# Optimization experiments

Hardware: AMD Instinct MI355X
Metric: run time of the kernel (lower is better)

The kernel has to match this reference:

```python
import jax, jax.numpy as jnp
import numpy as np

ROI_SIZE = 14  # hard-coded in the torch module


def _bilinear(feature, x, y):
    """feature: [B,C,H,W]; x, y: arbitrary (matching) shape S of sample coords.
    Returns [B, C, *S]. Matches torch code: corner indices are clamped BEFORE
    the interpolation weights are computed from them."""
    H, W = feature.shape[-2:]
    y1 = jnp.clip(jnp.floor(y).astype(jnp.int32), 0, H - 1)
    y2 = jnp.clip(jnp.floor(y).astype(jnp.int32) + 1, 0, H - 1)
    x1 = jnp.clip(jnp.floor(x).astype(jnp.int32), 0, W - 1)
    x2 = jnp.clip(jnp.floor(x).astype(jnp.int32) + 1, 0, W - 1)
    wx_lo = x - x1  # weight toward x2 column
    wx_hi = x2 - x  # weight toward x1 column
    wy_lo = y - y1
    wy_hi = y2 - y
    p = feature[:, :, y1, x1] * wx_hi + feature[:, :, y1, x2] * wx_lo
    q = feature[:, :, y2, x1] * wx_hi + feature[:, :, y2, x2] * wx_lo
    return p * wy_hi + q * wy_lo


def setup_inputs() -> dict:
    key = jax.random.key(0)
    kf, k1, k2, k3, k4 = jax.random.split(key, 5)
    B, C, H, W, R = 1, 256, 200, 320, 128
    feature = jax.random.normal(kf, (B, C, H, W), dtype=jnp.float32)
    y1 = jax.random.uniform(k1, (R,), minval=0.0, maxval=H * 0.5)
    x1 = jax.random.uniform(k2, (R,), minval=0.0, maxval=W * 0.5)
    hh = jax.random.uniform(k3, (R,), minval=8.0, maxval=H * 0.45)
    ww = jax.random.uniform(k4, (R,), minval=8.0, maxval=W * 0.45)
    rois = jnp.stack([y1, x1, y1 + hh, x1 + ww], axis=-1).astype(jnp.float32)
    return {"feature": feature, "rois": rois}


def reference(feature, rois):
    R = rois.shape[0]
    B, C, H, W = feature.shape
    sh = (rois[:, 2] - rois[:, 0]) / ROI_SIZE  # [R] bin height stride
    sw = (rois[:, 3] - rois[:, 1]) / ROI_SIZE  # [R] bin width stride
    m = jnp.arange(ROI_SIZE, dtype=rois.dtype)
    y_base = rois[:, 0:1] + sh[:, None] * m  # [R, M]
    x_base = rois[:, 1:2] + sw[:, None] * m  # [R, N]
    frac = jnp.array([1.0 / 3.0, 2.0 / 3.0], dtype=rois.dtype)
    ys = y_base[:, :, None] + sh[:, None, None] * frac  # [R, M, 2]
    xs = x_base[:, :, None] + sw[:, None, None] * frac  # [R, N, 2]
    # all 4 (y, x) sample-point combos per bin -> [R, M, N, 2, 2]
    yy = jnp.broadcast_to(ys[:, :, None, :, None], (R, ROI_SIZE, ROI_SIZE, 2, 2))
    xx = jnp.broadcast_to(xs[:, None, :, None, :], (R, ROI_SIZE, ROI_SIZE, 2, 2))
    samples = _bilinear(feature, xx, yy)  # [B, C, R, M, N, 2, 2]
    # Faithful to torch.max(tensor) with NO dim: global max over B, C, R and
    # the 4 sample points, giving one scalar per bin (m, n).
    bin_max = jnp.max(samples, axis=(0, 1, 2, 5, 6))  # [M, N]
    return jnp.broadcast_to(bin_max, (R, C, ROI_SIZE, ROI_SIZE))
```

## Files before the change

kernel.cpp:

```cpp
#include <hip/hip_runtime.h>
#include <float.h>

#define CC 256
#define HH 200
#define WW 320
#define HW (HH * WW)
#define MM 14
#define CG 8
#define CPB (CC / CG)
#define CPW (CPB / 4)

__global__ void roi_init(float* __restrict__ binmax) {
    int t = blockIdx.x * blockDim.x + threadIdx.x;
    if (t < MM * MM) binmax[t] = -FLT_MAX;
}

__device__ inline void atomicMaxF(float* addr, float val) {
    if (val >= 0.0f) {
        atomicMax((int*)addr, __float_as_int(val));
    } else {
        atomicMin((unsigned int*)addr, __float_as_uint(val));
    }
}

__global__ __launch_bounds__(256) void roi_reduce(
    const float* __restrict__ feature,
    const float* __restrict__ rois,
    float* __restrict__ binmax)
{
    __shared__ float pmax[4][MM];

    const int bid = blockIdx.x;
    const int cg  = bid & (CG - 1);
    const int rm  = bid >> 3;
    const int m   = rm % MM;
    const int r   = rm / MM;
    const int tid  = threadIdx.x;
    const int w    = tid >> 6;
    const int lane = tid & 63;

    const float ry1 = rois[r * 4 + 0];
    const float rx1 = rois[r * 4 + 1];
    const float ry2 = rois[r * 4 + 2];
    const float rx2 = rois[r * 4 + 3];
    const float sh = (ry2 - ry1) * (1.0f / 14.0f);
    const float sw = (rx2 - rx1) * (1.0f / 14.0f);
    const float f13 = 1.0f / 3.0f, f23 = 2.0f / 3.0f;

    const int s = lane & 31;
    const int i = lane >> 5;
    const int n = s >> 1;
    const int j = s & 1;
    const bool active = s < 28;

    const float x = rx1 + sw * (float)n + sw * (j ? f23 : f13);
    const float y = ry1 + sh * (float)m + sh * (i ? f23 : f13);
    const int x1c = min(max((int)floorf(x), 0), WW - 1);
    const int x2c = min(max((int)floorf(x) + 1, 0), WW - 1);
    const int y1c = min(max((int)floorf(y), 0), HH - 1);
    const int y2c = min(max((int)floorf(y) + 1, 0), HH - 1);
    const float wxlo = x - (float)x1c, wxhi = (float)x2c - x;
    const float wylo = y - (float)y1c, wyhi = (float)y2c - y;

    int o11 = y1c * WW + x1c;
    int o12 = y1c * WW + x2c;
    int o21 = y2c * WW + x1c;
    int o22 = y2c * WW + x2c;
    if (!active) { o11 = o12 = o21 = o22 = 0; }

    const float* fbase = feature + (cg * CPB + w * CPW) * HW;

    float v11[CPW], v12[CPW], v21[CPW], v22[CPW];
    #pragma unroll
    for (int c = 0; c < CPW; ++c) {
        const float* fc = fbase + c * HW;
        v11[c] = fc[o11];
        v12[c] = fc[o12];
        v21[c] = fc[o21];
        v22[c] = fc[o22];
    }

    float lmax = -FLT_MAX;
    #pragma unroll
    for (int c = 0; c < CPW; ++c) {
        float p = v11[c] * wxhi + v12[c] * wxlo;
        float q = v21[c] * wxhi + v22[c] * wxlo;
        lmax = fmaxf(lmax, p * wyhi + q * wylo);
    }

    float v = lmax;
    v = fmaxf(v, __shfl_xor(v, 1));
    v = fmaxf(v, __shfl_xor(v, 32));
    if (active && j == 0 && i == 0) pmax[w][n] = v;
    __syncthreads();
    if (tid < MM) {
        float vv = fmaxf(fmaxf(pmax[0][tid], pmax[1][tid]),
                         fmaxf(pmax[2][tid], pmax[3][tid]));
        atomicMaxF(&binmax[m * MM + tid], vv);
    }
}

#define BCAST_BLOCKS 784
__global__ __launch_bounds__(256) void roi_bcast(
    const float* __restrict__ binmax, float4* __restrict__ out, int total4)
{
    const int idx0 = blockIdx.x * 256 + threadIdx.x;
    const float4 val = ((const float4*)binmax)[idx0 % 49];
    const int stride = BCAST_BLOCKS * 256;
    #pragma unroll
    for (int k = 0; k < 8; ++k) {
        int idx = idx0 + k * stride;
        if (idx < total4) out[idx] = val;
    }
}

extern "C" void kernel_launch(void* const* d_in, const int* in_sizes, int n_in,
                              void* d_out, int out_size, void* d_ws, size_t ws_size,
                              hipStream_t stream) {
    const float* feature = (const float*)d_in[0];
    const float* rois    = (const float*)d_in[1];
    float* binmax = (float*)d_ws;
    float* out    = (float*)d_out;

    const int R = in_sizes[1] / 4;

    roi_init<<<1, 256, 0, stream>>>(binmax);
    roi_reduce<<<R * MM * CG, 256, 0, stream>>>(feature, rois, binmax);

    const int total4 = out_size / 4;
    roi_bcast<<<BCAST_BLOCKS, 256, 0, stream>>>(binmax, (float4*)out, total4);
}
```

Measured before the change: 152.5 us.

## Transpose feature to channels-last in workspace for coalesced bilinear gathers

Adds a tiled shared-memory transpose that rewrites the NCHW feature map into an HWC copy in the workspace. A new reduce kernel then gathers the bilinear corners as contiguous float4 channel vectors and processes all 14 rows of an ROI per block, replacing the channel-strided scalar gathers. The cost is an extra full read and write of the feature map on every call. The new path needs a workspace of roughly 65 MB and falls back to the old kernel when the workspace is smaller.

```diff
diff --git a/kernel.cpp b/kernel.cpp
--- a/kernel.cpp
+++ b/kernel.cpp
@@ -10,6 +10,9 @@
 #define CPB (CC / CG)
 #define CPW (CPB / 4)
 
+#define WS_FT_OFF 1024
+#define FT_BYTES ((size_t)HW * CC * 4)
+
 __global__ void roi_init(float* __restrict__ binmax) {
     int t = blockIdx.x * blockDim.x + threadIdx.x;
     if (t < MM * MM) binmax[t] = -FLT_MAX;
@@ -23,13 +26,132 @@
     }
 }
 
-__global__ __launch_bounds__(256) void roi_reduce(
+__global__ __launch_bounds__(256) void roi_transpose(
+    const float* __restrict__ f, float* __restrict__ ft)
+{
+    __shared__ float tile[64][65];
+    const int gb = blockIdx.x;
+    const int h  = gb / 20;
+    const int rest = gb % 20;
+    const int wb = (rest / 4) * 64;
+    const int cb = (rest % 4) * 64;
+    const int tx = threadIdx.x & 63;
+    const int g  = threadIdx.x >> 6;
+    #pragma unroll
+    for (int k = 0; k < 16; ++k) {
+        int cl = g * 16 + k;
+        tile[cl][tx] = f[(cb + cl) * HW + h * WW + wb + tx];
+    }
+    __syncthreads();
+    #pragma unroll
+    for (int k = 0; k < 16; ++k) {
+        int wl = g * 16 + k;
+        ft[(h * WW + wb + wl) * CC + cb + tx] = tile[tx][wl];
+    }
+}
+
+__global__ __launch_bounds__(256) void roi_reduce_t(
+    const float* __restrict__ ft,
+    const float* __restrict__ rois,
+    float* __restrict__ binmax)
+{
+    __shared__ float pm[MM][MM][2];
+
+    const int bid = blockIdx.x;
+    const int cg  = bid & (CG - 1);
+    const int r   = bid >> 3;
+    const int tid  = threadIdx.x;
+    const int w    = tid >> 6;
+    const int lane = tid & 63;
+    const int iw    = w & 1;
+    const int nbase = (w >> 1) * 7;
+    const int s8 = lane >> 3;
+    const int c8 = lane & 7;
+    const int cgo = cg * 8 + c8;
+
+    const float ry1 = rois[r * 4 + 0];
+    const float rx1 = rois[r * 4 + 1];
+    const float ry2 = rois[r * 4 + 2];
+    const float rx2 = rois[r * 4 + 3];
+    const float sh = (ry2 - ry1) * (1.0f / 14.0f);
+    const float sw = (rx2 - rx1) * (1.0f / 14.0f);
+    const float f13 = 1.0f / 3.0f, f23 = 2.0f / 3.0f;
+    const float yfrac = iw ? f23 : f13;
+
+    const float4* f4 = (const float4*)ft;
+
+    float wxlo[2], wxhi[2];
+    int ox1[2], ox2[2];
+    bool val[2];
+    #pragma unroll
+    for (int p = 0; p < 2; ++p) {
+        const int ls = p * 8 + s8;
+        val[p] = ls < 14;
+        const int n = nbase + (ls >> 1);
+        const int j = ls & 1;
+        const float x = rx1 + sw * (float)n + sw * (j ? f23 : f13);
+        const int x1c = min(max((int)floorf(x), 0), WW - 1);
+        const int x2c = min(max((int)floorf(x) + 1, 0), WW - 1);
+        wxlo[p] = x - (float)x1c;
+        wxhi[p] = (float)x2c - x;
+        ox1[p] = val[p] ? x1c : 0;
+        ox2[p] = val[p] ? x2c : 0;
+    }
+
+    for (int m = 0; m < MM; ++m) {
+        const float y = ry1 + sh * (float)m + sh * yfrac;
+        const int y1c = min(max((int)floorf(y), 0), HH - 1);
+        const int y2c = min(max((int)floorf(y) + 1, 0), HH - 1);
+        const float wylo = y - (float)y1c, wyhi = (float)y2c - y;
+        const int row1 = y1c * WW, row2 = y2c * WW;
+
+        float4 v11[2], v12[2], v21[2], v22[2];
+        #pragma unroll
+        for (int p = 0; p < 2; ++p) {
+            v11[p] = f4[(row1 + ox1[p]) * 64 + cgo];
+            v12[p] = f4[(row1 + ox2[p]) * 64 + cgo];
+            v21[p] = f4[(row2 + ox1[p]) * 64 + cgo];
+            v22[p] = f4[(row2 + ox2[p]) * 64 + cgo];
+        }
+        #pragma unroll
+        for (int p = 0; p < 2; ++p) {
+            float px = v11[p].x * wxhi[p] + v12[p].x * wxlo[p];
+            float py = v11[p].y * wxhi[p] + v12[p].y * wxlo[p];
+            float pz = v11[p].z * wxhi[p] + v12[p].z * wxlo[p];
+            float pw = v11[p].w * wxhi[p] + v12[p].w * wxlo[p];
+            float qx = v21[p].x * wxhi[p] + v22[p].x * wxlo[p];
+            float qy = v21[p].y * wxhi[p] + v22[p].y * wxlo[p];
+            float qz = v21[p].z * wxhi[p] + v22[p].z * wxlo[p];
+            float qw = v21[p].w * wxhi[p] + v22[p].w * wxlo[p];
+            float rx = px * wyhi + qx * wylo;
+            float ry = py * wyhi + qy * wylo;
+            float rz = pz * wyhi + qz * wylo;
+            float rw = pw * wyhi + qw * wylo;
+            float sm = fmaxf(fmaxf(rx, ry), fmaxf(rz, rw));
+            if (!val[p]) sm = -FLT_MAX;
+            sm = fmaxf(sm, __shfl_xor(sm, 1));
+            sm = fmaxf(sm, __shfl_xor(sm, 2));
+            sm = fmaxf(sm, __shfl_xor(sm, 4));
+            sm = fmaxf(sm, __shfl_xor(sm, 8));
+            const int ls = p * 8 + s8;
+            if ((lane & 15) == 0 && val[p])
+                pm[m][nbase + (ls >> 1)][iw] = sm;
+        }
+    }
+
+    __syncthreads();
+    if (tid < MM * MM) {
+        float vv = fmaxf(pm[tid / MM][tid % MM][0], pm[tid / MM][tid % MM][1]);
+        atomicMaxF(&binmax[tid], vv);
+    }
+}
+
+__global__ __launch_bounds__(256) void roi_reduce_g(
     const float* __restrict__ feature,
     const float* __restrict__ rois,
     float* __restrict__ binmax)
 {
     __shared__ float pmax[4][MM];
-
     const int bid = blockIdx.x;
     const int cg  = bid & (CG - 1);
     const int rm  = bid >> 3;
@@ -62,24 +184,17 @@
     const float wxlo = x - (float)x1c, wxhi = (float)x2c - x;
     const float wylo = y - (float)y1c, wyhi = (float)y2c - y;
 
-    int o11 = y1c * WW + x1c;
-    int o12 = y1c * WW + x2c;
-    int o21 = y2c * WW + x1c;
-    int o22 = y2c * WW + x2c;
+    int o11 = y1c * WW + x1c, o12 = y1c * WW + x2c;
+    int o21 = y2c * WW + x1c, o22 = y2c * WW + x2c;
     if (!active) { o11 = o12 = o21 = o22 = 0; }
 
     const float* fbase = feature + (cg * CPB + w * CPW) * HW;
-
     float v11[CPW], v12[CPW], v21[CPW], v22[CPW];
     #pragma unroll
     for (int c = 0; c < CPW; ++c) {
         const float* fc = fbase + c * HW;
-        v11[c] = fc[o11];
-        v12[c] = fc[o12];
-        v21[c] = fc[o21];
-        v22[c] = fc[o22];
-    }
-
+        v11[c] = fc[o11]; v12[c] = fc[o12]; v21[c] = fc[o21]; v22[c] = fc[o22];
+    }
     float lmax = -FLT_MAX;
     #pragma unroll
     for (int c = 0; c < CPW; ++c) {
@@ -87,7 +202,6 @@
         float q = v21[c] * wxhi + v22[c] * wxlo;
         lmax = fmaxf(lmax, p * wyhi + q * wylo);
     }
-
     float v = lmax;
     v = fmaxf(v, __shfl_xor(v, 1));
     v = fmaxf(v, __shfl_xor(v, 32));
@@ -125,7 +239,14 @@
     const int R = in_sizes[1] / 4;
 
     roi_init<<<1, 256, 0, stream>>>(binmax);
-    roi_reduce<<<R * MM * CG, 256, 0, stream>>>(feature, rois, binmax);
+
+    if (ws_size >= WS_FT_OFF + FT_BYTES) {
+        float* ft = (float*)((char*)d_ws + WS_FT_OFF);
+        roi_transpose<<<HH * (WW / 64) * (CC / 64), 256, 0, stream>>>(feature, ft);
+        roi_reduce_t<<<R * CG, 256, 0, stream>>>(ft, rois, binmax);
+    } else {
+        roi_reduce_g<<<R * MM * CG, 256, 0, stream>>>(feature, rois, binmax);
+    }
 
     const int total4 = out_size / 4;
     roi_bcast<<<BCAST_BLOCKS, 256, 0, stream>>>(binmax, (float4*)out, total4);
```

Measured after the change: 148.7 us. 2.5% less time.
